# Optimization experiments

Hardware: AMD Instinct MI355X
Metric: run time of the kernel (lower is better)

## Reference

```python
import jax, jax.numpy as jnp
import numpy as np

H = 32      # query heads
KV = 8      # kv heads
D = 128     # head_dim
HID = 4096
S = 4       # num sequences
L = 1024    # tokens per sequence
N = S * L   # total tokens
EPS = 1e-6
THETA = 10000.0
GROUPS = H // KV


def setup_inputs() -> dict:
    key = jax.random.key(0)
    ks = jax.random.split(key, 12)
    def w(k, shape, std):
        return jax.random.normal(k, shape, dtype=jnp.float32) * std
    return {
        "hidden": w(ks[0], (N, HID), 1.0),
        "mu_prev": w(ks[1], (N, HID), 1.0),
        "positions": jnp.tile(jnp.arange(L, dtype=jnp.int32), S),
        "Wq": w(ks[2], (H * D, HID), HID ** -0.5),
        "Wk": w(ks[3], (KV * D, HID), HID ** -0.5),
        "Wv": w(ks[4], (KV * D, HID), HID ** -0.5),
        "Wo": w(ks[5], (HID, H * D), (H * D) ** -0.5),
        "Wmq": w(ks[6], (H * D, HID), 0.01),
        "Wmk": w(ks[7], (KV * D, HID), 0.01),
        "Wmv": w(ks[8], (KV * D, HID), 0.01),
        "q_norm_w": jnp.ones((D,), jnp.float32),
        "k_norm_w": jnp.ones((D,), jnp.float32),
    }


def _rmsnorm(x, w):
    var = jnp.mean(jnp.square(x), axis=-1, keepdims=True)
    return x * jax.lax.rsqrt(var + EPS) * w


def _rope_cos_sin(positions):
    inv_freq = 1.0 / (THETA ** (jnp.arange(0, D, 2, dtype=jnp.float32) / D))  # [D/2]
    freqs = positions.astype(jnp.float32)[:, None] * inv_freq[None, :]        # [N, D/2]
    emb = jnp.concatenate([freqs, freqs], axis=-1)                            # [N, D]
    return jnp.cos(emb), jnp.sin(emb)


def _rotate_half(x):
    x1, x2 = jnp.split(x, 2, axis=-1)
    return jnp.concatenate([-x2, x1], axis=-1)


def _apply_rotary(x, cos, sin):
    # x: [N, h, D]; cos/sin: [N, D]
    return x * cos[:, None, :] + _rotate_half(x) * sin[:, None, :]


def reference(hidden, mu_prev, positions, Wq, Wk, Wv, Wo, Wmq, Wmk, Wmv, q_norm_w, k_norm_w):
    # QKV projections + mu-bias fusion
    q = hidden @ Wq.T + mu_prev @ Wmq.T     # [N, H*D]
    k = hidden @ Wk.T + mu_prev @ Wmk.T     # [N, KV*D]
    v = hidden @ Wv.T + mu_prev @ Wmv.T     # [N, KV*D]
    q = q.reshape(N, H, D)
    k = k.reshape(N, KV, D)
    v = v.reshape(N, KV, D)
    # QK RMSNorm
    q = _rmsnorm(q, q_norm_w)
    k = _rmsnorm(k, k_norm_w)
    # RoPE
    cos, sin = _rope_cos_sin(positions)
    q = _apply_rotary(q, cos, sin)
    k = _apply_rotary(k, cos, sin)
    # GQA: expand kv heads to match q heads
    k = jnp.repeat(k, GROUPS, axis=1)       # [N, H, D]
    v = jnp.repeat(v, GROUPS, axis=1)
    # Varlen causal attention: equal-length seqs -> batched [S, L, H, D]
    qs = q.reshape(S, L, H, D)
    ks = k.reshape(S, L, H, D)
    vs = v.reshape(S, L, H, D)
    scale = 1.0 / np.sqrt(D)
    scores = jnp.einsum("slhd,smhd->shlm", qs, ks) * scale   # [S, H, L, L]
    causal = jnp.tril(jnp.ones((L, L), dtype=bool))
    scores = jnp.where(causal, scores, jnp.finfo(scores.dtype).min)
    probs = jax.nn.softmax(scores, axis=-1)
    out = jnp.einsum("shlm,smhd->slhd", probs, vs)           # [S, L, H, D]
    out = out.reshape(N, H * D)
    return out @ Wo.T                                         # [N, HID]
```

## Files before the change

### kernel.cpp

```cpp
#include <hip/hip_runtime.h>
#include <hip/hip_bf16.h>
#include <stdint.h>

#define DEV static __device__ __forceinline__

typedef __bf16 bf16_t;
typedef __bf16 bf16x8 __attribute__((ext_vector_type(8)));
typedef __bf16 bf16x4 __attribute__((ext_vector_type(4)));
typedef float  f32x4  __attribute__((ext_vector_type(4)));


DEV void gload_lds16(const void* g, void* l) {
  __builtin_amdgcn_global_load_lds(
      (__attribute__((address_space(1))) void*)(uintptr_t)(g),
      (__attribute__((address_space(3))) void*)(uintptr_t)(l),
      16, 0, 0);
}

#define BARRIER() asm volatile("s_barrier" ::: "memory")
#define MFMA16(a, b, c) __builtin_amdgcn_mfma_f32_16x16x32_bf16((a), (b), (c), 0, 0, 0)

__global__ void k_pack_pair(const float* __restrict__ A, const float* __restrict__ B,
                            bf16_t* __restrict__ dst, int rows) {
  size_t n4 = (size_t)rows * 1024;
  size_t stride = (size_t)gridDim.x * blockDim.x;
  for (size_t i = (size_t)blockIdx.x * blockDim.x + threadIdx.x; i < n4; i += stride) {
    size_t r = i >> 10, c4 = i & 1023;
    float4 va = ((const float4*)A)[i];
    float4 vb = ((const float4*)B)[i];
    bf16x4 oa = { (bf16_t)va.x, (bf16_t)va.y, (bf16_t)va.z, (bf16_t)va.w };
    bf16x4 ob = { (bf16_t)vb.x, (bf16_t)vb.y, (bf16_t)vb.z, (bf16_t)vb.w };
    ((bf16x4*)dst)[r * 2048 + c4]        = oa;
    ((bf16x4*)dst)[r * 2048 + 1024 + c4] = ob;
  }
}

__global__ void k_convert(const float* __restrict__ A, bf16_t* __restrict__ dst, size_t n4) {
  size_t stride = (size_t)gridDim.x * blockDim.x;
  for (size_t i = (size_t)blockIdx.x * blockDim.x + threadIdx.x; i < n4; i += stride) {
    float4 v = ((const float4*)A)[i];
    bf16x4 o = { (bf16_t)v.x, (bf16_t)v.y, (bf16_t)v.z, (bf16_t)v.w };
    ((bf16x4*)dst)[i] = o;
  }
}

template<typename CT, int NSPLIT>
__global__ __launch_bounds__(512, 2) void k_gemm256(
    const bf16_t* __restrict__ A, const bf16_t* __restrict__ B,
    CT* __restrict__ C, int M, int N, int Kfull) {
  __shared__ __align__(16) char lds[131072];
  const int tid = threadIdx.x, lane = tid & 63, wid = tid >> 6;
  const int l15 = lane & 15, lhi = lane >> 4;
  const int wr = wid >> 2, wc = wid & 3;
  const int bid = blockIdx.x, nwg = gridDim.x;
  const int cpx = nwg >> 3;
  const int swz = (bid & 7) * cpx + (bid >> 3);
  const int nbn = N >> 8;
  const int tiles = (M >> 8) * nbn;
  const int ks = (NSPLIT > 1) ? (swz / tiles) : 0;
  const int t  = (NSPLIT > 1) ? (swz % tiles) : swz;
  const int bn = t % nbn, bm = t / nbn;
  const int Kloop = Kfull / NSPLIT;
  const int nkt = Kloop >> 6;

  const size_t rowK = (size_t)Kfull * 2;
  const size_t kbase = (size_t)ks * Kloop * 2;
  const int off0 = wid * 1024 + lane * 16, off1 = off0 + 8192;
  const int r0 = off0 >> 7, r1 = off1 >> 7;
  const int c0 = ((off0 >> 4) & 7) ^ (r0 & 7);
  const int c1 = ((off1 >> 4) & 7) ^ (r1 & 7);
  const char* sA0 = (const char*)A + ((size_t)bm * 256 + r0) * rowK + kbase + c0 * 16;
  const char* sA1 = (const char*)A + ((size_t)bm * 256 + r1) * rowK + kbase + c1 * 16;
  const char* sB0 = (const char*)B + ((size_t)bn * 256 + r0) * rowK + kbase + c0 * 16;
  const char* sB1 = (const char*)B + ((size_t)bn * 256 + r1) * rowK + kbase + c1 * 16;
  const size_t hstep = (size_t)128 * rowK;

  int ht = 0;
  const int htmax = nkt * 4;
  auto stage = [&]() {
    if (ht < htmax) {
      const int kt_s = ht >> 2, part = ht & 3, db = kt_s & 1, hf = part & 1;
      const size_t goff = (size_t)kt_s * 128 + (hf ? hstep : (size_t)0);
      char* ldst;
      const char *g0, *g1;
      if (part < 2) { ldst = lds + 65536 + (db * 2 + hf) * 16384; g0 = sB0 + goff; g1 = sB1 + goff; }
      else          { ldst = lds + (db * 2 + hf) * 16384;          g0 = sA0 + goff; g1 = sA1 + goff; }
      gload_lds16(g0, ldst + wid * 1024);
      gload_lds16(g1, ldst + 8192 + wid * 1024);
      ht++;
    }
  };

  f32x4 acc[8][4] = {};
  const int xr = l15 & 7;
  const int ck0 = (lhi ^ xr) * 8;
  const int ck1 = (((4 + lhi) ^ xr)) * 8;

  for (int i = 0; i < 7; ++i) stage();
  asm volatile("s_waitcnt vmcnt(6)" ::: "memory");
  BARRIER();

  for (int kt = 0; kt < nkt; ++kt) {
    const int d = kt & 1;
    const bf16_t* Asl = (const bf16_t*)(lds + (d * 2 + wr) * 16384);
    const bf16_t* Bsl = (const bf16_t*)(lds + 65536 + (d * 2 + (wc >> 1)) * 16384);
    bf16x8 a[4][2], b[4][2];
#pragma unroll
    for (int mi = 0; mi < 4; ++mi) {
      const int ro = (mi * 16 + l15) * 64;
      a[mi][0] = *(const bf16x8*)(Asl + ro + ck0);
      a[mi][1] = *(const bf16x8*)(Asl + ro + ck1);
    }
#pragma unroll
    for (int n = 0; n < 2; ++n) {
      const int ro = ((wc & 1) * 64 + n * 16 + l15) * 64;
      b[n][0] = *(const bf16x8*)(Bsl + ro + ck0);
      b[n][1] = *(const bf16x8*)(Bsl + ro + ck1);
    }
    stage();
    asm volatile("s_waitcnt lgkmcnt(8)" ::: "memory");
    BARRIER();
    __builtin_amdgcn_s_setprio(1);
#pragma unroll
    for (int mi = 0; mi < 4; ++mi)
#pragma unroll
      for (int ni = 0; ni < 2; ++ni) {
        acc[mi][ni] = MFMA16(a[mi][0], b[ni][0], acc[mi][ni]);
        acc[mi][ni] = MFMA16(a[mi][1], b[ni][1], acc[mi][ni]);
      }
    __builtin_amdgcn_s_setprio(0);
    BARRIER();
#pragma unroll
    for (int n = 2; n < 4; ++n) {
      const int ro = ((wc & 1) * 64 + n * 16 + l15) * 64;
      b[n][0] = *(const bf16x8*)(Bsl + ro + ck0);
      b[n][1] = *(const bf16x8*)(Bsl + ro + ck1);
    }
    stage();
    BARRIER();
    __builtin_amdgcn_s_setprio(1);
#pragma unroll
    for (int mi = 0; mi < 4; ++mi)
#pragma unroll
      for (int ni = 0; ni < 2; ++ni) {
        acc[mi][2 + ni] = MFMA16(a[mi][0], b[2 + ni][0], acc[mi][2 + ni]);
        acc[mi][2 + ni] = MFMA16(a[mi][1], b[2 + ni][1], acc[mi][2 + ni]);
      }
    __builtin_amdgcn_s_setprio(0);
    BARRIER();
#pragma unroll
    for (int mi = 0; mi < 4; ++mi) {
      const int ro = (64 + mi * 16 + l15) * 64;
      a[mi][0] = *(const bf16x8*)(Asl + ro + ck0);
      a[mi][1] = *(const bf16x8*)(Asl + ro + ck1);
    }
    stage();
    BARRIER();
    __builtin_amdgcn_s_setprio(1);
#pragma unroll
    for (int mi = 0; mi < 4; ++mi)
#pragma unroll
      for (int ni = 0; ni < 2; ++ni) {
        acc[4 + mi][ni] = MFMA16(a[mi][0], b[ni][0], acc[4 + mi][ni]);
        acc[4 + mi][ni] = MFMA16(a[mi][1], b[ni][1], acc[4 + mi][ni]);
      }
    __builtin_amdgcn_s_setprio(0);
    BARRIER();
    stage();
    BARRIER();
    __builtin_amdgcn_s_setprio(1);
#pragma unroll
    for (int mi = 0; mi < 4; ++mi)
#pragma unroll
      for (int ni = 0; ni < 2; ++ni) {
        acc[4 + mi][2 + ni] = MFMA16(a[mi][0], b[2 + ni][0], acc[4 + mi][2 + ni]);
        acc[4 + mi][2 + ni] = MFMA16(a[mi][1], b[2 + ni][1], acc[4 + mi][2 + ni]);
      }
    __builtin_amdgcn_s_setprio(0);
    if (kt >= nkt - 2) asm volatile("s_waitcnt vmcnt(0)" ::: "memory");
    else               asm volatile("s_waitcnt vmcnt(6)" ::: "memory");
    BARRIER();
  }

  CT* Cp = C + (size_t)ks * M * N;
#pragma unroll
  for (int m = 0; m < 8; ++m) {
    const int row0 = bm * 256 + wr * 128 + m * 16 + 4 * lhi;
#pragma unroll
    for (int n = 0; n < 4; ++n) {
      const int col = bn * 256 + wc * 64 + n * 16 + l15;
#pragma unroll
      for (int i = 0; i < 4; ++i)
        Cp[(size_t)(row0 + i) * N + col] = (CT)acc[m][n][i];
    }
  }
}

__global__ __launch_bounds__(256) void k_norm_rope(
    const bf16_t* __restrict__ qkvA, const bf16_t* __restrict__ qkvB,
    const int* __restrict__ pos,
    const float* __restrict__ qw, const float* __restrict__ kw,
    bf16_t* __restrict__ Q, bf16_t* __restrict__ Kk, bf16_t* __restrict__ V) {
  const int w = blockIdx.x * 4 + (threadIdx.x >> 6);
  const int lane = threadIdx.x & 63;
  const int n = w / 48, slot = w % 48;
  const bf16_t* rowA = qkvA + (size_t)n * 6144;
  const bf16_t* rowB = qkvB + (size_t)n * 6144;
  if (slot >= 40) {
    const int h2 = slot - 40;
    const int c = 5120 + h2 * 128 + lane;
    float x0 = (float)rowA[c] + (float)rowB[c];
    float x1 = (float)rowA[c + 64] + (float)rowB[c + 64];
    bf16_t* dst = V + ((size_t)n * 8 + h2) * 128;
    dst[lane] = (bf16_t)x0;
    dst[lane + 64] = (bf16_t)x1;
    return;
  }
  const bool isq = slot < 32;
  const int h = isq ? slot : slot - 32;
  const int coff = (isq ? h * 128 : 4096 + h * 128) + lane;
  float x0 = (float)rowA[coff] + (float)rowB[coff];
  float x1 = (float)rowA[coff + 64] + (float)rowB[coff + 64];
  float ss = x0 * x0 + x1 * x1;
#pragma unroll
  for (int m = 32; m; m >>= 1) ss += __shfl_xor(ss, m, 64);
  const float inv = rsqrtf(ss * (1.0f / 128.0f) + 1e-6f);
  const float* wgt = isq ? qw : kw;
  float y0 = x0 * inv * wgt[lane];
  float y1 = x1 * inv * wgt[lane + 64];
  const float ang = (float)pos[n] * expf((float)lane * -0.14391156608f);
  float sn, cs;
  sincosf(ang, &sn, &cs);
  float o0 = y0 * cs - y1 * sn;
  float o1 = y1 * cs + y0 * sn;
  bf16_t* dst = isq ? (Q + ((size_t)n * 32 + h) * 128) : (Kk + ((size_t)n * 8 + h) * 128);
  dst[lane] = (bf16_t)o0;
  dst[lane + 64] = (bf16_t)o1;
}

__global__ __launch_bounds__(256, 2) void k_attn(
    const bf16_t* __restrict__ Q, const bf16_t* __restrict__ Kk,
    const bf16_t* __restrict__ V, bf16_t* __restrict__ O) {
  __shared__ __align__(16) bf16_t Ks[64 * 128];
  __shared__ __align__(16) bf16_t Vt[128 * 72];
  __shared__ __align__(16) bf16_t Ps[4][32 * 72];
  const int b = blockIdx.x;
  const int qb = b & 7, h = (b >> 3) & 31, s = b >> 8;
  const int kvh = h >> 2;
  const int tid = threadIdx.x, lane = tid & 63, wid = tid >> 6;
  const int l15 = lane & 15, lhi = lane >> 4;

  bf16x8 qf[2][4];
  {
    const int qrow = qb * 128 + wid * 32;
#pragma unroll
    for (int mt = 0; mt < 2; mt++) {
      const size_t base = ((size_t)(s * 1024 + qrow + mt * 16 + l15) * 32 + h) * 128;
#pragma unroll
      for (int kc = 0; kc < 4; kc++)
        qf[mt][kc] = *(const bf16x8*)(Q + base + kc * 32 + 8 * lhi);
    }
  }
  f32x4 of[2][8] = {};
  float mx[2][4], li[2][4];
#pragma unroll
  for (int mt = 0; mt < 2; mt++)
#pragma unroll
    for (int i = 0; i < 4; i++) { mx[mt][i] = -1e30f; li[mt][i] = 0.f; }

  const int ktiles = (qb + 1) * 2;
  const int vr_base = tid >> 4;
  const int vd0 = (tid & 15) * 8;

  for (int kt = 0; kt < ktiles; kt++) {
    const int kv0 = kt * 64;
#pragma unroll
    for (int c = 0; c < 4; c++) {
      const int wb = wid * 4096 + c * 1024;
      const int o = wb + lane * 16;
      const int krow = o >> 8;
      const int ci = (o >> 4) & 15;
      const int cs = ci ^ (krow & 7);
      const char* src =
          (const char*)(Kk + ((size_t)(s * 1024 + kv0 + krow) * 8 + kvh) * 128) + cs * 16;
      gload_lds16(src, (char*)Ks + wb);
    }
#pragma unroll
    for (int c = 0; c < 4; c++) {
      const int r = c * 16 + vr_base;
      bf16x8 v = *(const bf16x8*)(V + ((size_t)(s * 1024 + kv0 + r) * 8 + kvh) * 128 + vd0);
#pragma unroll
      for (int j = 0; j < 8; j++) {
        const int d = vd0 + j;
        const int cc = (r >> 3) ^ ((d >> 3) & 7);
        Vt[d * 72 + cc * 8 + (r & 7)] = v[j];
      }
    }
    __syncthreads();

    f32x4 sf[2][4] = {};
#pragma unroll
    for (int kc = 0; kc < 4; kc++) {
      bf16x8 kf[4];
#pragma unroll
      for (int n = 0; n < 4; n++) {
        const int krow = n * 16 + l15;
        const int ci = (kc * 4 + lhi) ^ (krow & 7);
        kf[n] = *(const bf16x8*)(Ks + krow * 128 + ci * 8);
      }
#pragma unroll
      for (int mt = 0; mt < 2; mt++)
#pragma unroll
        for (int n = 0; n < 4; n++)
          sf[mt][n] = MFMA16(qf[mt][kc], kf[n], sf[mt][n]);
    }

    const bool masked = (kt >= 2 * qb);
    const float scale = 0.08838834764831845f;
    float pv[2][4][4];
#pragma unroll
    for (int mt = 0; mt < 2; mt++) {
#pragma unroll
      for (int i = 0; i < 4; i++) {
        float rm = -1e30f;
#pragma unroll
        for (int n = 0; n < 4; n++) {
          float sv = sf[mt][n][i] * scale;
          if (masked) {
            const int kvg = kv0 + n * 16 + l15;
            const int qg = qb * 128 + wid * 32 + mt * 16 + 4 * lhi + i;
            if (kvg > qg) sv = -1e30f;
          }
          pv[mt][n][i] = sv;
          rm = fmaxf(rm, sv);
        }
#pragma unroll
        for (int mm = 1; mm < 16; mm <<= 1) rm = fmaxf(rm, __shfl_xor(rm, mm, 64));
        const float nm = fmaxf(mx[mt][i], rm);
        float ts = 0.f;
#pragma unroll
        for (int n = 0; n < 4; n++) {
          float e = __expf(pv[mt][n][i] - nm);
          pv[mt][n][i] = e;
          ts += e;
        }
#pragma unroll
        for (int mm = 1; mm < 16; mm <<= 1) ts += __shfl_xor(ts, mm, 64);
        const float al = __expf(mx[mt][i] - nm);
        li[mt][i] = li[mt][i] * al + ts;
        mx[mt][i] = nm;
#pragma unroll
        for (int n = 0; n < 8; n++) of[mt][n][i] *= al;
      }
    }

    bf16_t* myP = &Ps[wid][0];
#pragma unroll
    for (int mt = 0; mt < 2; mt++)
#pragma unroll
      for (int n = 0; n < 4; n++)
#pragma unroll
        for (int i = 0; i < 4; i++)
          myP[(mt * 16 + 4 * lhi + i) * 72 + n * 16 + l15] = (bf16_t)pv[mt][n][i];

#pragma unroll
    for (int kc = 0; kc < 2; kc++) {
      bf16x8 pf[2];
#pragma unroll
      for (int mt = 0; mt < 2; mt++)
        pf[mt] = *(const bf16x8*)(myP + (mt * 16 + l15) * 72 + kc * 32 + 8 * lhi);
#pragma unroll
      for (int n = 0; n < 8; n++) {
        const int d = n * 16 + l15;
        const int cc = (kc * 4 + lhi) ^ ((d >> 3) & 7);
        bf16x8 vf = *(const bf16x8*)(Vt + d * 72 + cc * 8);
#pragma unroll
        for (int mt = 0; mt < 2; mt++)
          of[mt][n] = MFMA16(pf[mt], vf, of[mt][n]);
      }
    }
    __syncthreads();
  }

#pragma unroll
  for (int mt = 0; mt < 2; mt++) {
#pragma unroll
    for (int i = 0; i < 4; i++) {
      const float invl = 1.0f / li[mt][i];
      const int tokrow = qb * 128 + wid * 32 + mt * 16 + 4 * lhi + i;
      bf16_t* dst = O + (size_t)(s * 1024 + tokrow) * 4096 + h * 128;
#pragma unroll
      for (int n = 0; n < 8; n++)
        dst[n * 16 + l15] = (bf16_t)(of[mt][n][i] * invl);
    }
  }
}

extern "C" void kernel_launch(void* const* d_in, const int* in_sizes, int n_in,
                              void* d_out, int out_size, void* d_ws, size_t ws_size,
                              hipStream_t stream) {
  const float* hidden = (const float*)d_in[0];
  const float* mu     = (const float*)d_in[1];
  const int*   pos    = (const int*)d_in[2];
  const float* Wq  = (const float*)d_in[3];
  const float* Wk  = (const float*)d_in[4];
  const float* Wv  = (const float*)d_in[5];
  const float* Wo  = (const float*)d_in[6];
  const float* Wmq = (const float*)d_in[7];
  const float* Wmk = (const float*)d_in[8];
  const float* Wmv = (const float*)d_in[9];
  const float* qw  = (const float*)d_in[10];
  const float* kw  = (const float*)d_in[11];
  float* out = (float*)d_out;
  char* ws = (char*)d_ws;

  if (ws_size < 301989888u) return;

  bf16_t* Wqkv = (bf16_t*)(ws);
  bf16_t* Wob  = (bf16_t*)(ws + 100663296);
  bf16_t* Xb   = (bf16_t*)(ws + 134217728);
  bf16_t* Qb   = (bf16_t*)(ws + 134217728);
  bf16_t* Kb   = (bf16_t*)(ws + 167772160);
  bf16_t* Vb   = (bf16_t*)(ws + 176160768);
  bf16_t* qkvA = (bf16_t*)(ws + 201326592);
  bf16_t* qkvB = (bf16_t*)(ws + 251658240);
  bf16_t* Ob   = (bf16_t*)(ws + 201326592);

  k_pack_pair<<<2048, 256, 0, stream>>>(hidden, mu, Xb, 4096);
  k_pack_pair<<<2048, 256, 0, stream>>>(Wq, Wmq, Wqkv, 4096);
  k_pack_pair<<<1024, 256, 0, stream>>>(Wk, Wmk, Wqkv + (size_t)4096 * 8192, 1024);
  k_pack_pair<<<1024, 256, 0, stream>>>(Wv, Wmv, Wqkv + (size_t)5120 * 8192, 1024);
  k_convert<<<2048, 256, 0, stream>>>(Wo, Wob, (size_t)4096 * 4096 / 4);

  k_gemm256<bf16_t, 2><<<768, 512, 0, stream>>>(Xb, Wqkv, qkvA, 4096, 6144, 8192);
  k_norm_rope<<<49152, 256, 0, stream>>>(qkvA, qkvB, pos, qw, kw, Qb, Kb, Vb);
  k_attn<<<1024, 256, 0, stream>>>(Qb, Kb, Vb, Ob);
  k_gemm256<float, 1><<<256, 512, 0, stream>>>(Ob, Wob, out, 4096, 4096, 4096);
}
```

Baseline: 849.6 us.

## Fuse conversion kernels, unroll GEMM main loop by two, swap tile order

Merges the five fp32-to-bf16 pack/convert launches into a single grid-stride kernel, which removes launch overhead and tail gaps between small kernels. The GEMM's lambda-based staging with runtime slot computation is replaced by a manually double-unrolled loop with fixed LDS slots, a peeled epilogue, and a register temp for each accumulator. The aim is to cut index arithmetic and branches in the hot loop. Tile mapping now walks M fastest instead of N, changing which tiles share L2 reuse of the weight operand. This risks different cache behaviour and assumes nkt is even.

```diff
diff --git a/kernel.cpp b/kernel.cpp
--- a/kernel.cpp
+++ b/kernel.cpp
@@ -20,27 +20,41 @@
 #define BARRIER() asm volatile("s_barrier" ::: "memory")
 #define MFMA16(a, b, c) __builtin_amdgcn_mfma_f32_16x16x32_bf16((a), (b), (c), 0, 0, 0)
 
-__global__ void k_pack_pair(const float* __restrict__ A, const float* __restrict__ B,
-                            bf16_t* __restrict__ dst, int rows) {
-  size_t n4 = (size_t)rows * 1024;
+DEV void pack_pair_chunk(const float* __restrict__ A, const float* __restrict__ B,
+                         bf16_t* __restrict__ dst, size_t i) {
+  size_t r = i >> 10, c = i & 1023;
+  float4 va = ((const float4*)A)[i];
+  float4 vb = ((const float4*)B)[i];
+  bf16x4 oa = {(bf16_t)va.x, (bf16_t)va.y, (bf16_t)va.z, (bf16_t)va.w};
+  bf16x4 ob = {(bf16_t)vb.x, (bf16_t)vb.y, (bf16_t)vb.z, (bf16_t)vb.w};
+  ((bf16x4*)dst)[r * 2048 + c] = oa;
+  ((bf16x4*)dst)[r * 2048 + 1024 + c] = ob;
+}
+
+__global__ void k_pack_all(const float* __restrict__ hidden, const float* __restrict__ mu,
+                           const float* __restrict__ Wq, const float* __restrict__ Wmq,
+                           const float* __restrict__ Wk, const float* __restrict__ Wmk,
+                           const float* __restrict__ Wv, const float* __restrict__ Wmv,
+                           const float* __restrict__ Wo,
+                           bf16_t* __restrict__ Xb, bf16_t* __restrict__ Wqkv,
+                           bf16_t* __restrict__ Wob) {
+  const size_t t0 = 4194304, t1 = 8388608, t2 = 9437184, t3 = 10485760, t4 = 14680064;
   size_t stride = (size_t)gridDim.x * blockDim.x;
-  for (size_t i = (size_t)blockIdx.x * blockDim.x + threadIdx.x; i < n4; i += stride) {
-    size_t r = i >> 10, c4 = i & 1023;
-    float4 va = ((const float4*)A)[i];
-    float4 vb = ((const float4*)B)[i];
-    bf16x4 oa = { (bf16_t)va.x, (bf16_t)va.y, (bf16_t)va.z, (bf16_t)va.w };
-    bf16x4 ob = { (bf16_t)vb.x, (bf16_t)vb.y, (bf16_t)vb.z, (bf16_t)vb.w };
-    ((bf16x4*)dst)[r * 2048 + c4]        = oa;
-    ((bf16x4*)dst)[r * 2048 + 1024 + c4] = ob;
-  }
-}
-
-__global__ void k_convert(const float* __restrict__ A, bf16_t* __restrict__ dst, size_t n4) {
-  size_t stride = (size_t)gridDim.x * blockDim.x;
-  for (size_t i = (size_t)blockIdx.x * blockDim.x + threadIdx.x; i < n4; i += stride) {
-    float4 v = ((const float4*)A)[i];
-    bf16x4 o = { (bf16_t)v.x, (bf16_t)v.y, (bf16_t)v.z, (bf16_t)v.w };
-    ((bf16x4*)dst)[i] = o;
+  for (size_t i = (size_t)blockIdx.x * blockDim.x + threadIdx.x; i < t4; i += stride) {
+    if (i < t0) {
+      pack_pair_chunk(hidden, mu, Xb, i);
+    } else if (i < t1) {
+      pack_pair_chunk(Wq, Wmq, Wqkv, i - t0);
+    } else if (i < t2) {
+      pack_pair_chunk(Wk, Wmk, Wqkv + (size_t)4096 * 8192, i - t1);
+    } else if (i < t3) {
+      pack_pair_chunk(Wv, Wmv, Wqkv + (size_t)5120 * 8192, i - t2);
+    } else {
+      size_t j = i - t3;
+      float4 v = ((const float4*)Wo)[j];
+      bf16x4 o = {(bf16_t)v.x, (bf16_t)v.y, (bf16_t)v.z, (bf16_t)v.w};
+      ((bf16x4*)Wob)[j] = o;
+    }
   }
 }
 
@@ -55,11 +69,11 @@
   const int bid = blockIdx.x, nwg = gridDim.x;
   const int cpx = nwg >> 3;
   const int swz = (bid & 7) * cpx + (bid >> 3);
-  const int nbn = N >> 8;
-  const int tiles = (M >> 8) * nbn;
+  const int nbm = M >> 8;
+  const int tiles = nbm * (N >> 8);
   const int ks = (NSPLIT > 1) ? (swz / tiles) : 0;
   const int t  = (NSPLIT > 1) ? (swz % tiles) : swz;
-  const int bn = t % nbn, bm = t / nbn;
+  const int bm = t % nbm, bn = t / nbm;
   const int Kloop = Kfull / NSPLIT;
   const int nkt = Kloop >> 6;
 
@@ -73,114 +87,117 @@
   const char* sA1 = (const char*)A + ((size_t)bm * 256 + r1) * rowK + kbase + c1 * 16;
   const char* sB0 = (const char*)B + ((size_t)bn * 256 + r0) * rowK + kbase + c0 * 16;
   const char* sB1 = (const char*)B + ((size_t)bn * 256 + r1) * rowK + kbase + c1 * 16;
-  const size_t hstep = (size_t)128 * rowK;
-
-  int ht = 0;
-  const int htmax = nkt * 4;
-  auto stage = [&]() {
-    if (ht < htmax) {
-      const int kt_s = ht >> 2, part = ht & 3, db = kt_s & 1, hf = part & 1;
-      const size_t goff = (size_t)kt_s * 128 + (hf ? hstep : (size_t)0);
-      char* ldst;
-      const char *g0, *g1;
-      if (part < 2) { ldst = lds + 65536 + (db * 2 + hf) * 16384; g0 = sB0 + goff; g1 = sB1 + goff; }
-      else          { ldst = lds + (db * 2 + hf) * 16384;          g0 = sA0 + goff; g1 = sA1 + goff; }
-      gload_lds16(g0, ldst + wid * 1024);
-      gload_lds16(g1, ldst + 8192 + wid * 1024);
-      ht++;
-    }
-  };
+  const size_t hst = (size_t)128 * rowK;
+
+  enum { A0S = 0, A1S = 16384, A2S = 32768, A3S = 49152,
+         B0S = 65536, B1S = 81920, B2S = 98304, B3S = 114688 };
+
+#define STG(slot, pa, pb, off) do { \
+    gload_lds16((pa) + (off), lds + (slot) + wid * 1024); \
+    gload_lds16((pb) + (off), lds + (slot) + 8192 + wid * 1024); } while (0)
+
+  const bf16_t* Ae = (const bf16_t*)(lds + A0S + wr * 16384);
+  const bf16_t* Be = (const bf16_t*)(lds + B0S + (wc >> 1) * 16384);
+  const bf16_t* Ao = (const bf16_t*)(lds + A2S + wr * 16384);
+  const bf16_t* Bo = (const bf16_t*)(lds + B2S + (wc >> 1) * 16384);
+  const int bro = (wc & 1) * 64;
 
   f32x4 acc[8][4] = {};
+  bf16x8 a[4][2], b[4][2];
   const int xr = l15 & 7;
   const int ck0 = (lhi ^ xr) * 8;
-  const int ck1 = (((4 + lhi) ^ xr)) * 8;
-
-  for (int i = 0; i < 7; ++i) stage();
+  const int ck1 = ((4 + lhi) ^ xr) * 8;
+
+#define RD_A(base, rb) do { _Pragma("unroll") \
+    for (int mi = 0; mi < 4; ++mi) { \
+      const int ro = ((rb) + mi * 16 + l15) * 64; \
+      a[mi][0] = *(const bf16x8*)((base) + ro + ck0); \
+      a[mi][1] = *(const bf16x8*)((base) + ro + ck1); } } while (0)
+#define RD_B(base) do { _Pragma("unroll") \
+    for (int n = 0; n < 4; ++n) { \
+      const int ro = (bro + n * 16 + l15) * 64; \
+      b[n][0] = *(const bf16x8*)((base) + ro + ck0); \
+      b[n][1] = *(const bf16x8*)((base) + ro + ck1); } } while (0)
+#define MM(qm, qn) do { _Pragma("unroll") \
+    for (int mi = 0; mi < 4; ++mi) { _Pragma("unroll") \
+      for (int ni = 0; ni < 2; ++ni) { \
+        f32x4 t_ = acc[(qm) * 4 + mi][(qn) * 2 + ni]; \
+        t_ = MFMA16(a[mi][0], b[(qn) * 2 + ni][0], t_); \
+        t_ = MFMA16(a[mi][1], b[(qn) * 2 + ni][1], t_); \
+        acc[(qm) * 4 + mi][(qn) * 2 + ni] = t_; } } } while (0)
+#define PRIO_MM(qm, qn) do { __builtin_amdgcn_s_setprio(1); MM(qm, qn); \
+    __builtin_amdgcn_s_setprio(0); } while (0)
+
+  STG(B0S, sB0, sB1, 0);
+  STG(B1S, sB0, sB1, hst);
+  STG(A0S, sA0, sA1, 0);
+  STG(A1S, sA0, sA1, hst);
+  STG(B2S, sB0, sB1, 128);
+  STG(B3S, sB0, sB1, 128 + hst);
+  STG(A2S, sA0, sA1, 128);
   asm volatile("s_waitcnt vmcnt(6)" ::: "memory");
   BARRIER();
 
-  for (int kt = 0; kt < nkt; ++kt) {
-    const int d = kt & 1;
-    const bf16_t* Asl = (const bf16_t*)(lds + (d * 2 + wr) * 16384);
-    const bf16_t* Bsl = (const bf16_t*)(lds + 65536 + (d * 2 + (wc >> 1)) * 16384);
-    bf16x8 a[4][2], b[4][2];
-#pragma unroll
-    for (int mi = 0; mi < 4; ++mi) {
-      const int ro = (mi * 16 + l15) * 64;
-      a[mi][0] = *(const bf16x8*)(Asl + ro + ck0);
-      a[mi][1] = *(const bf16x8*)(Asl + ro + ck1);
-    }
-#pragma unroll
-    for (int n = 0; n < 2; ++n) {
-      const int ro = ((wc & 1) * 64 + n * 16 + l15) * 64;
-      b[n][0] = *(const bf16x8*)(Bsl + ro + ck0);
-      b[n][1] = *(const bf16x8*)(Bsl + ro + ck1);
-    }
-    stage();
+  size_t g = 0;
+  for (int ktp = 0; ktp < nkt / 2 - 1; ++ktp) {
+    RD_A(Ae, 0); RD_B(Be);
+    STG(A3S, sA0, sA1, g + 128 + hst);
     asm volatile("s_waitcnt lgkmcnt(8)" ::: "memory");
     BARRIER();
-    __builtin_amdgcn_s_setprio(1);
-#pragma unroll
-    for (int mi = 0; mi < 4; ++mi)
-#pragma unroll
-      for (int ni = 0; ni < 2; ++ni) {
-        acc[mi][ni] = MFMA16(a[mi][0], b[ni][0], acc[mi][ni]);
-        acc[mi][ni] = MFMA16(a[mi][1], b[ni][1], acc[mi][ni]);
-      }
-    __builtin_amdgcn_s_setprio(0);
-    BARRIER();
-#pragma unroll
-    for (int n = 2; n < 4; ++n) {
-      const int ro = ((wc & 1) * 64 + n * 16 + l15) * 64;
-      b[n][0] = *(const bf16x8*)(Bsl + ro + ck0);
-      b[n][1] = *(const bf16x8*)(Bsl + ro + ck1);
-    }
-    stage();
-    BARRIER();
-    __builtin_amdgcn_s_setprio(1);
-#pragma unroll
-    for (int mi = 0; mi < 4; ++mi)
-#pragma unroll
-      for (int ni = 0; ni < 2; ++ni) {
-        acc[mi][2 + ni] = MFMA16(a[mi][0], b[2 + ni][0], acc[mi][2 + ni]);
-        acc[mi][2 + ni] = MFMA16(a[mi][1], b[2 + ni][1], acc[mi][2 + ni]);
-      }
-    __builtin_amdgcn_s_setprio(0);
-    BARRIER();
-#pragma unroll
-    for (int mi = 0; mi < 4; ++mi) {
-      const int ro = (64 + mi * 16 + l15) * 64;
-      a[mi][0] = *(const bf16x8*)(Asl + ro + ck0);
-      a[mi][1] = *(const bf16x8*)(Asl + ro + ck1);
-    }
-    stage();
-    BARRIER();
-    __builtin_amdgcn_s_setprio(1);
-#pragma unroll
-    for (int mi = 0; mi < 4; ++mi)
-#pragma unroll
-      for (int ni = 0; ni < 2; ++ni) {
-        acc[4 + mi][ni] = MFMA16(a[mi][0], b[ni][0], acc[4 + mi][ni]);
-        acc[4 + mi][ni] = MFMA16(a[mi][1], b[ni][1], acc[4 + mi][ni]);
-      }
-    __builtin_amdgcn_s_setprio(0);
-    BARRIER();
-    stage();
-    BARRIER();
-    __builtin_amdgcn_s_setprio(1);
-#pragma unroll
-    for (int mi = 0; mi < 4; ++mi)
-#pragma unroll
-      for (int ni = 0; ni < 2; ++ni) {
-        acc[4 + mi][2 + ni] = MFMA16(a[mi][0], b[2 + ni][0], acc[4 + mi][2 + ni]);
-        acc[4 + mi][2 + ni] = MFMA16(a[mi][1], b[2 + ni][1], acc[4 + mi][2 + ni]);
-      }
-    __builtin_amdgcn_s_setprio(0);
-    if (kt >= nkt - 2) asm volatile("s_waitcnt vmcnt(0)" ::: "memory");
-    else               asm volatile("s_waitcnt vmcnt(6)" ::: "memory");
-    BARRIER();
-  }
+    PRIO_MM(0, 0);
+    BARRIER();
+    STG(B0S, sB0, sB1, g + 256);
+    BARRIER();
+    PRIO_MM(0, 1);
+    BARRIER();
+    RD_A(Ae, 64);
+    STG(B1S, sB0, sB1, g + 256 + hst);
+    BARRIER();
+    PRIO_MM(1, 0);
+    BARRIER();
+    STG(A0S, sA0, sA1, g + 256);
+    BARRIER();
+    PRIO_MM(1, 1);
+    asm volatile("s_waitcnt vmcnt(6)" ::: "memory");
+    BARRIER();
+    RD_A(Ao, 0); RD_B(Bo);
+    STG(A1S, sA0, sA1, g + 256 + hst);
+    asm volatile("s_waitcnt lgkmcnt(8)" ::: "memory");
+    BARRIER();
+    PRIO_MM(0, 0);
+    BARRIER();
+    STG(B2S, sB0, sB1, g + 384);
+    BARRIER();
+    PRIO_MM(0, 1);
+    BARRIER();
+    RD_A(Ao, 64);
+    STG(B3S, sB0, sB1, g + 384 + hst);
+    BARRIER();
+    PRIO_MM(1, 0);
+    BARRIER();
+    STG(A2S, sA0, sA1, g + 384);
+    BARRIER();
+    PRIO_MM(1, 1);
+    asm volatile("s_waitcnt vmcnt(6)" ::: "memory");
+    BARRIER();
+    g += 256;
+  }
+  RD_A(Ae, 0); RD_B(Be);
+  STG(A3S, sA0, sA1, g + 128 + hst);
+  BARRIER();
+  PRIO_MM(0, 0);
+  PRIO_MM(0, 1);
+  RD_A(Ae, 64);
+  PRIO_MM(1, 0);
+  PRIO_MM(1, 1);
+  asm volatile("s_waitcnt vmcnt(0)" ::: "memory");
+  BARRIER();
+  RD_A(Ao, 0); RD_B(Bo);
+  PRIO_MM(0, 0);
+  PRIO_MM(0, 1);
+  RD_A(Ao, 64);
+  PRIO_MM(1, 0);
+  PRIO_MM(1, 1);
 
   CT* Cp = C + (size_t)ks * M * N;
 #pragma unroll
@@ -194,6 +211,11 @@
         Cp[(size_t)(row0 + i) * N + col] = (CT)acc[m][n][i];
     }
   }
+#undef STG
+#undef RD_A
+#undef RD_B
+#undef MM
+#undef PRIO_MM
 }
 
 __global__ __launch_bounds__(256) void k_norm_rope(
@@ -426,12 +448,8 @@
   bf16_t* qkvB = (bf16_t*)(ws + 251658240);
   bf16_t* Ob   = (bf16_t*)(ws + 201326592);
 
-  k_pack_pair<<<2048, 256, 0, stream>>>(hidden, mu, Xb, 4096);
-  k_pack_pair<<<2048, 256, 0, stream>>>(Wq, Wmq, Wqkv, 4096);
-  k_pack_pair<<<1024, 256, 0, stream>>>(Wk, Wmk, Wqkv + (size_t)4096 * 8192, 1024);
-  k_pack_pair<<<1024, 256, 0, stream>>>(Wv, Wmv, Wqkv + (size_t)5120 * 8192, 1024);
-  k_convert<<<2048, 256, 0, stream>>>(Wo, Wob, (size_t)4096 * 4096 / 4);
-
+  k_pack_all<<<2048, 256, 0, stream>>>(hidden, mu, Wq, Wmq, Wk, Wmk, Wv, Wmv, Wo,
+                                       Xb, Wqkv, Wob);
   k_gemm256<bf16_t, 2><<<768, 512, 0, stream>>>(Xb, Wqkv, qkvA, 4096, 6144, 8192);
   k_norm_rope<<<49152, 256, 0, stream>>>(qkvA, qkvB, pos, qw, kw, Qb, Kb, Vb);
   k_attn<<<1024, 256, 0, stream>>>(Qb, Kb, Vb, Ob);
```

New measurement: 783.4 us. 1.08x faster.
